# Optimization experiments

Hardware: AMD Instinct MI355X
Metric: run time of the kernel (lower is better)

Reference implementation:

```python
import jax, jax.numpy as jnp
import numpy as np

N_HEADS = 8
N_POINTS = 4
EPS = 1e-5


def _conv1x1(x, w, b):
    # x: [B,C,H,W], w: [O,C]
    return jnp.einsum('bchw,oc->bohw', x, w) + b[None, :, None, None]


def _gn(x, g, b, groups=32):
    B, C, H, W = x.shape
    xr = x.reshape(B, groups, C // groups, H, W)
    m = xr.mean((2, 3, 4), keepdims=True)
    v = xr.var((2, 3, 4), keepdims=True)
    xn = ((xr - m) * jax.lax.rsqrt(v + EPS)).reshape(B, C, H, W)
    return xn * g[None, :, None, None] + b[None, :, None, None]


def _ln(x, g, b):
    m = x.mean(-1, keepdims=True)
    v = x.var(-1, keepdims=True)
    return (x - m) * jax.lax.rsqrt(v + EPS) * g + b


def _ln_spec(x, g2, b2, n):
    # modality-specific LayerNorm: separate params for v tokens [:n] and i tokens [n:]
    return jnp.concatenate([_ln(x[:, :n], g2[0], b2[0]), _ln(x[:, n:], g2[1], b2[1])], 1)


def _sine_pos(h, w, d):
    nf = d // 2
    scale = 2.0 * np.pi
    ye = jnp.arange(1, h + 1, dtype=jnp.float32) / h * scale
    xe = jnp.arange(1, w + 1, dtype=jnp.float32) / w * scale
    dim_t = 10000.0 ** (2.0 * (jnp.arange(nf) // 2).astype(jnp.float32) / nf)
    def enc(e):
        p = e[:, None] / dim_t
        return jnp.stack([jnp.sin(p[:, 0::2]), jnp.cos(p[:, 1::2])], -1).reshape(e.shape[0], nf)
    py = enc(ye)  # [h,nf]
    px = enc(xe)  # [w,nf]
    pos = jnp.concatenate([jnp.broadcast_to(py[:, None, :], (h, w, nf)),
                           jnp.broadcast_to(px[None, :, :], (h, w, nf))], -1)
    return pos.reshape(h * w, d)


def _bilinear(vl, loc):
    # vl: [B,h,w,Hd,Dh] value for one level, loc: [B,Lq,Hd,P,2] normalized (x,y)
    B, h, w, Hd, Dh = vl.shape
    Lq, P = loc.shape[1], loc.shape[3]
    x = loc[..., 0] * w - 0.5
    y = loc[..., 1] * h - 0.5
    x0 = jnp.floor(x)
    y0 = jnp.floor(y)
    wx = x - x0
    wy = y - y0
    x0i = x0.astype(jnp.int32)
    y0i = y0.astype(jnp.int32)
    v2 = vl.reshape(B, h * w, Hd, Dh).transpose(0, 2, 1, 3)  # [B,Hd,HW,Dh]
    def g(ix, iy):
        valid = ((ix >= 0) & (ix < w) & (iy >= 0) & (iy < h)).astype(vl.dtype)
        flat = jnp.clip(iy, 0, h - 1) * w + jnp.clip(ix, 0, w - 1)  # [B,Lq,Hd,P]
        idx = flat.transpose(0, 2, 1, 3).reshape(B, Hd, Lq * P)
        gv = jnp.take_along_axis(v2, idx[..., None], axis=2)  # [B,Hd,Lq*P,Dh]
        gv = gv.reshape(B, Hd, Lq, P, Dh).transpose(0, 2, 1, 3, 4)  # [B,Lq,Hd,P,Dh]
        return gv * valid[..., None]
    return (g(x0i, y0i) * ((1 - wx) * (1 - wy))[..., None]
            + g(x0i + 1, y0i) * (wx * (1 - wy))[..., None]
            + g(x0i, y0i + 1) * ((1 - wx) * wy)[..., None]
            + g(x0i + 1, y0i + 1) * (wx * wy)[..., None])


def _deform_attn(q, src, ref, shapes, ow, ob, aww, awb, vw, vb, opw, opb):
    B, Len, D = src.shape
    L = len(shapes)
    Hd, P = N_HEADS, N_POINTS
    Dh = D // Hd
    value = src @ vw + vb
    off = (q @ ow + ob).reshape(B, Len, Hd, L, P, 2)
    aw = jax.nn.softmax((q @ aww + awb).reshape(B, Len, Hd, L * P), -1).reshape(B, Len, Hd, L, P)
    norm = jnp.array([[s[1], s[0]] for s in shapes], jnp.float32)  # (w,h) per level
    loc = ref[None, :, None, None, None, :] + off / norm[None, None, None, :, None, :]
    out = jnp.zeros((B, Len, Hd, Dh), value.dtype)
    start = 0
    for l, (hh, ww) in enumerate(shapes):
        vl = value[:, start:start + hh * ww].reshape(B, hh, ww, Hd, Dh)
        samp = _bilinear(vl, loc[:, :, :, l])  # [B,Len,Hd,P,Dh]
        out = out + (samp * aw[:, :, :, l, :, None]).sum(3)
        start += hh * ww
    return out.reshape(B, Len, D) @ opw + opb


def _forward(input_v, input_i, av_w, av_b, av_g, av_be, ai_w, ai_b, ai_g, ai_be,
             level_embed, off_w, off_b, aw_w, aw_b, vp_w, vp_b, op_w, op_b,
             ln1_g, ln1_b, ffn1_w, ffn1_b, ffn2_w, ffn2_b, ln2_g, ln2_b,
             as_w, as_b, as_g, as_be):
    b, c, h, w = input_v.shape
    D = av_w.shape[0]
    hw = h * w
    fv = _gn(_conv1x1(input_v, av_w, av_b), av_g, av_be)
    fi = _gn(_conv1x1(input_i, ai_w, ai_b), ai_g, ai_be)
    sv = fv.reshape(b, D, hw).transpose(0, 2, 1)
    si = fi.reshape(b, D, hw).transpose(0, 2, 1)
    src = jnp.concatenate([sv, si], 1)  # [b, 2hw, D]
    pos = _sine_pos(h, w, D)
    posf = jnp.concatenate([pos + level_embed[0], pos + level_embed[1]], 0)
    gx = (jnp.arange(w, dtype=jnp.float32) + 0.5) / w
    gy = (jnp.arange(h, dtype=jnp.float32) + 0.5) / h
    X, Y = jnp.meshgrid(gx, gy)
    ref1 = jnp.stack([X, Y], -1).reshape(hw, 2)
    ref = jnp.concatenate([ref1, ref1], 0)  # [2hw, 2]
    shapes = [(h, w), (h, w)]
    for i in range(off_w.shape[0]):
        q = src + posf
        attn = _deform_attn(q, src, ref, shapes, off_w[i], off_b[i], aw_w[i], aw_b[i],
                            vp_w[i], vp_b[i], op_w[i], op_b[i])
        src = _ln_spec(src + attn, ln1_g[i], ln1_b[i], hw)
        ff = jax.nn.relu(src @ ffn1_w[i] + ffn1_b[i]) @ ffn2_w[i] + ffn2_b[i]
        src = _ln_spec(src + ff, ln2_g[i], ln2_b[i], hw)
    out = src[:, :hw] + src[:, hw:]  # chunk along tokens, sum modalities
    out = out.transpose(0, 2, 1).reshape(b, D, h, w)
    return _gn(_conv1x1(out, as_w, as_b), as_g, as_be)


def setup_inputs():
    key = jax.random.key(0)
    B, C, H, W = 16, 768, 20, 20
    D, NL, Hd, L, P, Dff = 512, 6, N_HEADS, 2, N_POINTS, 1024
    ks = iter(jax.random.split(key, 64))
    def rn(shape, scale=0.02):
        return jax.random.normal(next(ks), shape, jnp.float32) * scale
    return {
        'input_v': jax.random.normal(next(ks), (B, C, H, W), jnp.float32),
        'input_i': jax.random.normal(next(ks), (B, C, H, W), jnp.float32),
        'av_w': rn((D, C)), 'av_b': jnp.zeros((D,)), 'av_g': jnp.ones((D,)), 'av_be': jnp.zeros((D,)),
        'ai_w': rn((D, C)), 'ai_b': jnp.zeros((D,)), 'ai_g': jnp.ones((D,)), 'ai_be': jnp.zeros((D,)),
        'level_embed': rn((L, D)),
        'off_w': rn((NL, D, Hd * L * P * 2)), 'off_b': rn((NL, Hd * L * P * 2), 0.5),
        'aw_w': rn((NL, D, Hd * L * P)), 'aw_b': jnp.zeros((NL, Hd * L * P)),
        'vp_w': rn((NL, D, D)), 'vp_b': jnp.zeros((NL, D)),
        'op_w': rn((NL, D, D)), 'op_b': jnp.zeros((NL, D)),
        'ln1_g': jnp.ones((NL, 2, D)), 'ln1_b': jnp.zeros((NL, 2, D)),
        'ffn1_w': rn((NL, D, Dff)), 'ffn1_b': jnp.zeros((NL, Dff)),
        'ffn2_w': rn((NL, Dff, D)), 'ffn2_b': jnp.zeros((NL, D)),
        'ln2_g': jnp.ones((NL, 2, D)), 'ln2_b': jnp.zeros((NL, 2, D)),
        'as_w': rn((C, D)), 'as_b': jnp.zeros((C,)), 'as_g': jnp.ones((C,)), 'as_be': jnp.zeros((C,)),
    }


def reference(input_v, input_i, av_w, av_b, av_g, av_be, ai_w, ai_b, ai_g, ai_be,
              level_embed, off_w, off_b, aw_w, aw_b, vp_w, vp_b, op_w, op_b,
              ln1_g, ln1_b, ffn1_w, ffn1_b, ffn2_w, ffn2_b, ln2_g, ln2_b,
              as_w, as_b, as_g, as_be):
    return _forward(input_v, input_i, av_w, av_b, av_g, av_be, ai_w, ai_b, ai_g, ai_be,
                    level_embed, off_w, off_b, aw_w, aw_b, vp_w, vp_b, op_w, op_b,
                    ln1_g, ln1_b, ffn1_w, ffn1_b, ffn2_w, ffn2_b, ln2_g, ln2_b,
                    as_w, as_b, as_g, as_be)
```

## Files before the change

kernel.cpp:

```cpp
#include <hip/hip_runtime.h>
#include <hip/hip_bf16.h>
#include <cstddef>
#include <math.h>


constexpr int kB   = 16;
constexpr int kCin = 768;
constexpr int kHW  = 400;
constexpr int kWpx = 20;
constexpr int kHpx = 20;
constexpr int kD   = 512;
constexpr int kLen = 800;
constexpr int kDff = 1024;
constexpr int kNL  = 6;
constexpr float kEps = 1e-5f;

typedef __attribute__((ext_vector_type(8))) short s8v;
typedef __attribute__((ext_vector_type(4))) short s4v;
typedef __attribute__((ext_vector_type(4))) float f4v;

__device__ __forceinline__ int swzk(int row, int k) {
  return (k & ~31) | ((((k >> 3) + (row >> 1)) & 3) << 3) | (k & 7);
}

__device__ __forceinline__ unsigned short f2b(float f) {
  union { __hip_bfloat16 h; unsigned short u; } cv;
  cv.h = __float2bfloat16(f);
  return cv.u;
}

__device__ __forceinline__ float b2f(unsigned short u) {
  return __uint_as_float(((unsigned)u) << 16);
}

__device__ __forceinline__ void gll(const unsigned short* g, unsigned short* l) {
  __builtin_amdgcn_global_load_lds(
      (const __attribute__((address_space(1))) unsigned int*)g,
      (__attribute__((address_space(3))) unsigned int*)l, 16, 0, 0);
}

__device__ __forceinline__ void breduce2(float& s, float& s2, float* sh) {
#pragma unroll
  for (int o = 32; o > 0; o >>= 1) {
    s  += __shfl_down(s, o);
    s2 += __shfl_down(s2, o);
  }
  const int wid = threadIdx.x >> 6, lane = threadIdx.x & 63;
  if (lane == 0) { sh[wid] = s; sh[4 + wid] = s2; }
  __syncthreads();
  if (threadIdx.x == 0) {
    sh[0] = sh[0] + sh[1] + sh[2] + sh[3];
    sh[4] = sh[4] + sh[5] + sh[6] + sh[7];
  }
  __syncthreads();
  s = sh[0]; s2 = sh[4];
}

template<int EPI>
__global__ __launch_bounds__(256)
void mgemm(const unsigned short* __restrict__ Abf,
           const unsigned short* __restrict__ Bw,
           const float* __restrict__ bias,
           const unsigned short* __restrict__ resb,
           float* __restrict__ Cf, unsigned short* __restrict__ Cb2,
           const float* __restrict__ aux,
           unsigned short* __restrict__ Cb,
           int K, int ldc, int Nreal)
{
  __shared__ unsigned short As[3][4096];
  __shared__ unsigned short Bs[3][4096];
  const int tid = threadIdx.x;
  const int w = tid >> 6, l = tid & 63;

  const int gx = gridDim.x;
  const int nwg = gx * gridDim.y;
  const int bid = blockIdx.y * gx + blockIdx.x;
  const int q = nwg >> 3, r = nwg & 7;
  const int xcd = bid & 7, idx = bid >> 3;
  const int wgid = (xcd < r ? xcd * (q + 1) : r * (q + 1) + (xcd - r) * q) + idx;
  const int m0 = (wgid / gx) * 128;
  const int n0 = (wgid % gx) * 128;

  if (EPI == 6 && m0 >= 6400) { Bw = resb; bias = aux; }

  f4v acc[4][4] = {};

  const int srow = w * 32 + (l >> 2);
  const unsigned short* ga0 = Abf + (size_t)(m0 + srow) * K + (l & 3) * 8;
  const unsigned short* ga1 = ga0 + (size_t)16 * K;
  const unsigned short* gb0 = Bw + (size_t)(n0 + srow) * K + (l & 3) * 8;
  const unsigned short* gb1 = gb0 + (size_t)16 * K;
  const int lb0 = (w * 32) * 32;
  const int lb1 = (w * 32 + 16) * 32;

  int aoff[4], boff[4];
#pragma unroll
  for (int f = 0; f < 4; f++) {
    const int ra = (w >> 1) * 64 + f * 16 + (l & 15);
    aoff[f] = ra * 32 + ((((l >> 4) + (ra >> 1)) & 3) << 3);
    const int rb = (w & 1) * 64 + f * 16 + (l & 15);
    boff[f] = rb * 32 + ((((l >> 4) + (rb >> 1)) & 3) << 3);
  }

#define STAGE(ko, bi) do { \
    gll(ga0 + (ko), &As[bi][lb0]); gll(ga1 + (ko), &As[bi][lb1]); \
    gll(gb0 + (ko), &Bs[bi][lb0]); gll(gb1 + (ko), &Bs[bi][lb1]); } while (0)

  const int NT = K >> 5;
  STAGE(0, 0);
  STAGE(32, 1);

  int cur = 0;
  int bpre = 2;
  int kpre = 64;
  for (int t = 0; t < NT; ++t) {
    if (t + 1 < NT) asm volatile("s_waitcnt vmcnt(4)" ::: "memory");
    else            asm volatile("s_waitcnt vmcnt(0)" ::: "memory");
    __builtin_amdgcn_s_barrier();
    __builtin_amdgcn_sched_barrier(0);
    if (t + 2 < NT) STAGE(kpre, bpre);
    s8v af[4], bf4[4];
#pragma unroll
    for (int f = 0; f < 4; f++) {
      af[f]  = *(const s8v*)&As[cur][aoff[f]];
      bf4[f] = *(const s8v*)&Bs[cur][boff[f]];
    }
    __builtin_amdgcn_s_setprio(1);
#pragma unroll
    for (int i = 0; i < 4; i++)
#pragma unroll
      for (int j = 0; j < 4; j++)
        acc[i][j] = __builtin_amdgcn_mfma_f32_16x16x32_bf16(af[i], bf4[j], acc[i][j], 0, 0, 0);
    __builtin_amdgcn_s_setprio(0);
    kpre += 32;
    bpre = (bpre == 2) ? 0 : bpre + 1;
    cur  = (cur == 2) ? 0 : cur + 1;
  }
#undef STAGE

  const int colb = n0 + (w & 1) * 64;
  const int rowb = m0 + (w >> 1) * 64 + (l >> 4) * 4;
#pragma unroll
  for (int i = 0; i < 4; i++) {
#pragma unroll
    for (int j = 0; j < 4; j++) {
      const int col = colb + j * 16 + (l & 15);
      float bv;
      if (EPI == 4) bv = (col < kD) ? bias[col] : 0.0f;
      else          bv = bias[col];
#pragma unroll
      for (int r2 = 0; r2 < 4; r2++) {
        const int row = rowb + i * 16 + r2;
        float v = acc[i][j][r2] + bv;
        if (EPI == 1) {
          Cb[(size_t)row * ldc + swzk(row, col)] = f2b(fmaxf(v, 0.0f));
        } else if (EPI == 2) {
          v += b2f(resb[(size_t)row * kD + swzk(row, col)]);
          Cb[(size_t)row * kD + col] = f2b(v);
        } else if (EPI == 3) {
          const int bb = row / kHW, p = row % kHW;
          Cf[((size_t)bb * Nreal + col) * kHW + p] = v;
        } else if (EPI == 4) {
          if (col < kD) {
            Cb[(size_t)row * kD + col] = f2b(v);
          } else {
            const int c = col - kD;
            if (c < 192)
              Cb2[(size_t)row * 192 + c] = f2b(v + aux[(size_t)(row % kLen) * 192 + c]);
          }
        } else if (EPI == 5) {
          if (row < kLen) {
            const int ll = col >> 8, c = col & 255;
            if (c < 192)
              Cf[(((size_t)ll * kLen) + row) * 192 + c] = v;
          }
        } else {
          Cb[(size_t)row * kD + col] = f2b(v);
        }
      }
    }
  }
}

__device__ __forceinline__ void cvt8t(const float* __restrict__ W,
                                      unsigned short* __restrict__ out,
                                      int K, int N, int g)
{
  const int n = g % N;
  const int k = (g / N) * 8;
  s8v p;
#pragma unroll
  for (int j = 0; j < 8; j++) p[j] = (short)f2b(W[(size_t)(k + j) * N + n]);
  const int base = n * K + (k & ~31) + ((((k >> 3) + (n >> 1)) & 3) << 3);
  *(s8v*)&out[base] = p;
}

__global__ __launch_bounds__(256)
void cvt_all_k(const float* __restrict__ vp_w, const float* __restrict__ op_w,
               const float* __restrict__ off_w, const float* __restrict__ aw_w,
               const float* __restrict__ f1w_a, const float* __restrict__ f2w_a,
               unsigned short* __restrict__ wall)
{
  const int lyr = blockIdx.x / 832;
  int g = (blockIdx.x % 832) * 256 + threadIdx.x;
  unsigned short* wl = wall + (size_t)lyr * 1703936;
  if (g < 32768) { cvt8t(vp_w + (size_t)lyr * kD * kD, wl, 512, 512, g); return; }
  g -= 32768;
  if (g < 16384) {
    const int n = g & 255;
    const int k = (g >> 8) * 8;
    const float* ow  = off_w + (size_t)lyr * kD * 128;
    const float* aww = aw_w  + (size_t)lyr * kD * 64;
    s8v p;
#pragma unroll
    for (int j = 0; j < 8; j++) {
      float v = 0.0f;
      if (n < 128)      v = ow[(size_t)(k + j) * 128 + n];
      else if (n < 192) v = aww[(size_t)(k + j) * 64 + (n - 128)];
      p[j] = (short)f2b(v);
    }
    const int row = 512 + n;
    const int base = row * 512 + (k & ~31) + ((((k >> 3) + (row >> 1)) & 3) << 3);
    *(s8v*)&wl[base] = p;
    return;
  }
  g -= 16384;
  if (g < 32768) { cvt8t(op_w + (size_t)lyr * kD * kD, wl + 393216, 512, 512, g); return; }
  g -= 32768;
  if (g < 65536) { cvt8t(f1w_a + (size_t)lyr * kD * kDff, wl + 655360, 512, 1024, g); return; }
  g -= 65536;
  cvt8t(f2w_a + (size_t)lyr * kDff * kD, wl + 1179648, 1024, 512, g);
}

__global__ __launch_bounds__(256)
void pre_k(const float* __restrict__ level_embed,
           const float* __restrict__ off_w, const float* __restrict__ aw_w,
           const float* __restrict__ off_b, const float* __restrict__ aw_b,
           unsigned short* __restrict__ posfb,
           unsigned short* __restrict__ woaw_all, float* __restrict__ biasall)
{
  int g = blockIdx.x * 256 + threadIdx.x;
  if (g < 57344) {
    const int d0 = (g & 63) * 8;
    const int t  = g >> 6;
    s8v o;
    if (t >= kLen) {
#pragma unroll
      for (int j = 0; j < 8; j++) o[j] = 0;
    } else {
      const int lvl = t / kHW;
      const int tt = t % kHW;
      const int yy = tt / kWpx, xx = tt % kWpx;
#pragma unroll
      for (int j = 0; j < 8; j++) {
        const int d = d0 + j;
        const int dd = d & 255;
        const float e = (d < 256) ? ((float)(yy + 1) * (6.283185307179586f / kHpx))
                                  : ((float)(xx + 1) * (6.283185307179586f / kWpx));
        const float dimt = powf(10000.0f, (float)(dd >> 1) / 128.0f);
        const float pp = e / dimt;
        const float val = (dd & 1) ? cosf(pp) : sinf(pp);
        o[j] = (short)f2b(val + level_embed[lvl * kD + d]);
      }
    }
    *(s8v*)&posfb[(size_t)t * kD + swzk(t, d0)] = o;
    return;
  }
  g -= 57344;
  if (g < 98304) {
    const int l = g >> 14;
    const int gg = g & 16383;
    const int n = gg & 255;
    const int k = (gg >> 8) * 8;
    const float* ow = off_w + (size_t)l * kD * 128;
    const float* aww = aw_w + (size_t)l * kD * 64;
    s8v p;
#pragma unroll
    for (int j = 0; j < 8; j++) {
      float v = 0.0f;
      if (n < 128)      v = ow[(size_t)(k + j) * 128 + n];
      else if (n < 192) v = aww[(size_t)(k + j) * 64 + (n - 128)];
      p[j] = (short)f2b(v);
    }
    const int row = l * 256 + n;
    const int base = row * 512 + (k & ~31) + ((((k >> 3) + (row >> 1)) & 3) << 3);
    *(s8v*)&woaw_all[base] = p;
    return;
  }
  g -= 98304;
  if (g < 1536) {
    const int l = g >> 8, c = g & 255;
    float v = 0.0f;
    if (c < 128)      v = off_b[l * 128 + c];
    else if (c < 192) v = aw_b[l * 64 + (c - 128)];
    biasall[l * 256 + c] = v;
  }
}

__global__ void cvtw_d_k(const float* __restrict__ W, unsigned short* __restrict__ out,
                         int K, int N)
{
  const int gid = blockIdx.x * 256 + threadIdx.x;
  const int K8 = K >> 3;
  const int n  = gid / K8;
  const int k  = (gid % K8) * 8;
  s8v p;
#pragma unroll
  for (int j = 0; j < 8; j++) p[j] = (short)f2b(W[(size_t)n * K + k + j]);
  const int base = n * K + (k & ~31) + ((((k >> 3) + (n >> 1)) & 3) << 3);
  *(s8v*)&out[base] = p;
}

__global__ void tincvt_k(const float* __restrict__ inv, const float* __restrict__ ini,
                         const float* __restrict__ W0, const float* __restrict__ W1,
                         unsigned short* __restrict__ out, unsigned short* __restrict__ wcs)
{
  __shared__ float t[16][17];
  const int bid = blockIdx.x;
  if (bid < 38400) {
    const int z = bid / 1200;
    const int rem = bid % 1200;
    const int c0 = (rem % 48) * 16, p0 = (rem / 48) * 16;
    const int mod = z >> 4, b = z & 15;
    const float* in = (mod ? ini : inv) + (size_t)b * kCin * kHW;
    const int tx = threadIdx.x & 15, ty = threadIdx.x >> 4;
    t[ty][tx] = in[((size_t)(c0 + ty)) * kHW + p0 + tx];
    __syncthreads();
    const int row = z * kHW + p0 + ty;
    const int c = c0 + tx;
    out[(size_t)row * kCin + swzk(row, c)] = f2b(t[tx][ty]);
    return;
  }
  int gid = (bid - 38400) * 256 + threadIdx.x;
  const float* W = W0;
  unsigned short* o = wcs;
  if (gid >= 49152) { gid -= 49152; W = W1; o = wcs + 393216; }
  const int n = gid / 96;
  const int k = (gid % 96) * 8;
  s8v p;
#pragma unroll
  for (int j = 0; j < 8; j++) p[j] = (short)f2b(W[(size_t)n * kCin + k + j]);
  const int base = n * kCin + (k & ~31) + ((((k >> 3) + (n >> 1)) & 3) << 3);
  *(s8v*)&o[base] = p;
}

__global__ __launch_bounds__(256)
void gn_stats_tok_k(const unsigned short* __restrict__ x, float* __restrict__ stats)
{
  __shared__ float sh[8];
  const int mb = blockIdx.x >> 5;
  const int g = blockIdx.x & 31;
  const unsigned short* xb = x + (size_t)mb * kHW * kD + g * 16;
  float s = 0.f, s2 = 0.f;
  for (int i = threadIdx.x; i < 800; i += 256) {
    const int p = i >> 1, half = i & 1;
    const s8v u = *(const s8v*)&xb[(size_t)p * kD + half * 8];
#pragma unroll
    for (int j = 0; j < 8; j++) {
      const float v = b2f((unsigned short)u[j]);
      s += v; s2 += v * v;
    }
  }
  breduce2(s, s2, sh);
  if (threadIdx.x == 0) {
    const float mean = s / (kHW * 16.0f);
    const float var  = s2 / (kHW * 16.0f) - mean * mean;
    stats[blockIdx.x * 2]     = mean;
    stats[blockIdx.x * 2 + 1] = rsqrtf(var + kEps);
  }
}

__global__ void gn_norm_tok_k(const unsigned short* __restrict__ x,
                              unsigned short* __restrict__ srcb,
                              const float* __restrict__ stats,
                              const float* __restrict__ gv, const float* __restrict__ bev,
                              const float* __restrict__ gi, const float* __restrict__ bei)
{
  const int gid = blockIdx.x * 256 + threadIdx.x;
  const int d0 = (gid & 63) * 8;
  const int rl = gid >> 6;
  const int mb = rl / kHW;
  const int p  = rl - mb * kHW;
  const int mod = mb >> 4, b = mb & 15;
  const int g = d0 >> 4;
  const float mean = stats[(mb * 32 + g) * 2];
  const float rstd = stats[(mb * 32 + g) * 2 + 1];
  const float* gam = mod ? gi : gv;
  const float* bet = mod ? bei : bev;
  const s8v u = *(const s8v*)&x[(size_t)rl * kD + d0];
  const int row = b * kLen + mod * kHW + p;
  s8v o;
#pragma unroll
  for (int j = 0; j < 8; j++)
    o[j] = (short)f2b((b2f((unsigned short)u[j]) - mean) * rstd * gam[d0 + j] + bet[d0 + j]);
  *(s8v*)&srcb[(size_t)row * kD + swzk(row, d0)] = o;
}

__global__ __launch_bounds__(256)
void gn_stats_ch_k(const float* __restrict__ x, float* __restrict__ stats)
{
  __shared__ float sh[8];
  const int b = blockIdx.x >> 5;
  const int g = blockIdx.x & 31;
  const float* xb = x + (size_t)b * kCin * kHW + (size_t)g * 24 * kHW;
  float s = 0.f, s2 = 0.f;
  for (int i = threadIdx.x; i < 24 * kHW; i += 256) {
    const float v = xb[i];
    s += v; s2 += v * v;
  }
  breduce2(s, s2, sh);
  if (threadIdx.x == 0) {
    const float mean = s / (24.0f * kHW);
    const float var  = s2 / (24.0f * kHW) - mean * mean;
    stats[blockIdx.x * 2]     = mean;
    stats[blockIdx.x * 2 + 1] = rsqrtf(var + kEps);
  }
}

__global__ void gn_norm_ch_k(const float* __restrict__ x, float* __restrict__ out,
                             const float* __restrict__ stats,
                             const float* __restrict__ gam, const float* __restrict__ bet)
{
  const int idx = blockIdx.x * 256 + threadIdx.x;
  const int rest = idx / kHW;
  const int c = rest % kCin;
  const int b = rest / kCin;
  const int g = c / 24;
  const float mean = stats[(b * 32 + g) * 2];
  const float rstd = stats[(b * 32 + g) * 2 + 1];
  out[idx] = (x[idx] - mean) * rstd * gam[c] + bet[c];
}

__global__ __launch_bounds__(256)
void ln4_k(const unsigned short* __restrict__ x, unsigned short* __restrict__ outb,
           const float* __restrict__ gamma, const float* __restrict__ beta)
{
  const int row = blockIdx.x * 4 + (threadIdx.x >> 6);
  const int l = threadIdx.x & 63;
  const int mod = ((row % kLen) < kHW) ? 0 : 1;
  const s8v u = *(const s8v*)&x[(size_t)row * kD + l * 8];
  float v[8];
#pragma unroll
  for (int j = 0; j < 8; j++) v[j] = b2f((unsigned short)u[j]);
  float s = 0.f, s2 = 0.f;
#pragma unroll
  for (int j = 0; j < 8; j++) { s += v[j]; s2 += v[j] * v[j]; }
#pragma unroll
  for (int o = 32; o > 0; o >>= 1) {
    s  += __shfl_xor(s, o);
    s2 += __shfl_xor(s2, o);
  }
  const float mean = s * (1.0f / kD);
  const float var  = s2 * (1.0f / kD) - mean * mean;
  const float rstd = rsqrtf(var + kEps);
  const float* g  = gamma + mod * kD + l * 8;
  const float* be = beta  + mod * kD + l * 8;
  s8v o8;
#pragma unroll
  for (int j = 0; j < 8; j++)
    o8[j] = (short)f2b((v[j] - mean) * rstd * g[j] + be[j]);
  *(s8v*)&outb[(size_t)row * kD + swzk(row, l * 8)] = o8;
}

__global__ __launch_bounds__(256)
void sample_k(const unsigned short* __restrict__ value,
              const unsigned short* __restrict__ offaw,
              unsigned short* __restrict__ out)
{
  __shared__ float wls[2][64][8];
  const int tid = threadIdx.x;
  const int tok = tid >> 7;
  const int wt  = tid & 127;
  const int token = blockIdx.x * 2 + tok;
  const int b = token / kLen;
  const int t = token % kLen;
  const int tt = t % kHW;

  if (wt < 64) {
    const int h = wt >> 3, lp = wt & 7, lvl = lp >> 2, p = lp & 3;
    const unsigned short* oa = offaw + (size_t)token * 192;
    const float lg = b2f(oa[128 + h * 8 + lp]);
    float mx = lg;
#pragma unroll
    for (int msk = 1; msk < 8; msk <<= 1) mx = fmaxf(mx, __shfl_xor(mx, msk));
    const float ex = __expf(lg - mx);
    float ssum = ex;
#pragma unroll
    for (int msk = 1; msk < 8; msk <<= 1) ssum += __shfl_xor(ssum, msk);
    const float aw = ex / ssum;

    const float x = (float)(tt % kWpx) + b2f(oa[h * 16 + lvl * 8 + p * 2]);
    const float y = (float)(tt / kWpx) + b2f(oa[h * 16 + lvl * 8 + p * 2 + 1]);
    const float x0f = floorf(x), y0f = floorf(y);
    const float wx = x - x0f, wy = y - y0f;
    const int x0 = (int)x0f, y0 = (int)y0f;
    const int rowbase = b * kLen + lvl * kHW;
#pragma unroll
    for (int dy = 0; dy < 2; dy++) {
#pragma unroll
      for (int dx = 0; dx < 2; dx++) {
        const int ix = x0 + dx, iy = y0 + dy;
        const bool valid = (ix >= 0) & (ix < kWpx) & (iy >= 0) & (iy < kHpx);
        const float cw = (dx ? wx : 1.0f - wx) * (dy ? wy : 1.0f - wy);
        const float w = valid ? aw * cw : 0.0f;
        const int ixc = min(max(ix, 0), kWpx - 1);
        const int iyc = min(max(iy, 0), kHpx - 1);
        const int r = rowbase + iyc * kWpx + ixc;
        const int cn = dy * 2 + dx;
        wls[tok][wt][cn * 2]     = w;
        wls[tok][wt][cn * 2 + 1] = __int_as_float(r);
      }
    }
  }
  __syncthreads();

  const int c0 = wt * 4;
  const int h = wt >> 4;
  float acc0 = 0.f, acc1 = 0.f, acc2 = 0.f, acc3 = 0.f;
  const unsigned short* vb = value + c0;
#pragma unroll
  for (int pp = 0; pp < 8; pp++) {
    const float* wl = wls[tok][h * 8 + pp];
#pragma unroll
    for (int cn = 0; cn < 4; cn++) {
      const float w = wl[cn * 2];
      const int r = __float_as_int(wl[cn * 2 + 1]);
      const s4v q = *(const s4v*)(vb + (size_t)r * kD);
      acc0 += w * b2f((unsigned short)q[0]);
      acc1 += w * b2f((unsigned short)q[1]);
      acc2 += w * b2f((unsigned short)q[2]);
      acc3 += w * b2f((unsigned short)q[3]);
    }
  }
  const int sk = swzk(token, c0);
  s4v o;
  o[0] = (short)f2b(acc0); o[1] = (short)f2b(acc1);
  o[2] = (short)f2b(acc2); o[3] = (short)f2b(acc3);
  *(s4v*)&out[(size_t)token * kD + sk] = o;
}

__global__ void sumtok_k(const unsigned short* __restrict__ srcb,
                         unsigned short* __restrict__ tokb)
{
  const int gid = blockIdx.x * 256 + threadIdx.x;
  const int d0 = (gid & 63) * 8;
  const int rest = gid >> 6;
  const int b = rest / kHW, p = rest % kHW;
  const int r1 = b * kLen + p;
  const int r2 = r1 + kHW;
  const int ro = b * kHW + p;
  const s8v u1 = *(const s8v*)&srcb[(size_t)r1 * kD + swzk(r1, d0)];
  const s8v u2 = *(const s8v*)&srcb[(size_t)r2 * kD + swzk(r2, d0)];
  s8v o;
#pragma unroll
  for (int j = 0; j < 8; j++)
    o[j] = (short)f2b(b2f((unsigned short)u1[j]) + b2f((unsigned short)u2[j]));
  *(s8v*)&tokb[(size_t)ro * kD + swzk(ro, d0)] = o;
}

extern "C" void kernel_launch(void* const* d_in, const int* in_sizes, int n_in,
                              void* d_out, int out_size, void* d_ws, size_t ws_size,
                              hipStream_t stream)
{
  const float* input_v     = (const float*)d_in[0];
  const float* input_i     = (const float*)d_in[1];
  const float* av_w        = (const float*)d_in[2];
  const float* av_b        = (const float*)d_in[3];
  const float* av_g        = (const float*)d_in[4];
  const float* av_be       = (const float*)d_in[5];
  const float* ai_w        = (const float*)d_in[6];
  const float* ai_b        = (const float*)d_in[7];
  const float* ai_g        = (const float*)d_in[8];
  const float* ai_be       = (const float*)d_in[9];
  const float* level_embed = (const float*)d_in[10];
  const float* off_w       = (const float*)d_in[11];
  const float* off_b       = (const float*)d_in[12];
  const float* aw_w        = (const float*)d_in[13];
  const float* aw_b        = (const float*)d_in[14];
  const float* vp_w        = (const float*)d_in[15];
  const float* vp_b        = (const float*)d_in[16];
  const float* op_w        = (const float*)d_in[17];
  const float* op_b        = (const float*)d_in[18];
  const float* ln1_g       = (const float*)d_in[19];
  const float* ln1_b       = (const float*)d_in[20];
  const float* ffn1_w      = (const float*)d_in[21];
  const float* ffn1_b      = (const float*)d_in[22];
  const float* ffn2_w      = (const float*)d_in[23];
  const float* ffn2_b      = (const float*)d_in[24];
  const float* ln2_g       = (const float*)d_in[25];
  const float* ln2_b       = (const float*)d_in[26];
  const float* as_w        = (const float*)d_in[27];
  const float* as_b        = (const float*)d_in[28];
  const float* as_g        = (const float*)d_in[29];
  const float* as_be       = (const float*)d_in[30];

  unsigned short* offawb = (unsigned short*)d_ws;
  float* posWc   = (float*)(offawb + 2457600);
  float* biasall = posWc   + (size_t)921600;
  float* stats   = biasall + (size_t)1536;
  unsigned short* srcb     = (unsigned short*)(stats + 2048);
  unsigned short* bufA     = srcb     + (size_t)6553600;
  unsigned short* bufB     = bufA     + (size_t)13107200;
  unsigned short* wall     = bufB     + (size_t)6553600;
  unsigned short* wcs      = wall     + (size_t)10223616;
  unsigned short* woaw_all = wcs      + (size_t)786432;
  unsigned short* posfb    = woaw_all + (size_t)786432;
  float* wallf = (float*)wall;

  const int M = kB * kLen;

  pre_k<<<dim3(614), 256, 0, stream>>>(level_embed, off_w, aw_w, off_b, aw_b,
                                       posfb, woaw_all, biasall);
  mgemm<5><<<dim3(12, 7), 256, 0, stream>>>(
      posfb, woaw_all, biasall, nullptr, posWc, nullptr, nullptr, nullptr,
      512, 0, 0);

  tincvt_k<<<dim3(38784), 256, 0, stream>>>(input_v, input_i, av_w, ai_w,
                                            bufA, wcs);
  mgemm<6><<<dim3(4, 100), 256, 0, stream>>>(
      bufA, wcs, av_b, wcs + 393216, nullptr, nullptr, ai_b, bufB, 768, 512, 0);
  gn_stats_tok_k<<<dim3(1024), 256, 0, stream>>>(bufB, stats);
  gn_norm_tok_k<<<dim3(3200), 256, 0, stream>>>(
      bufB, srcb, stats, av_g, av_be, ai_g, ai_be);

  cvt_all_k<<<dim3(4992), 256, 0, stream>>>(vp_w, op_w, off_w, aw_w,
                                            ffn1_w, ffn2_w, wall);

  for (int l = 0; l < kNL; l++) {
    unsigned short* wcomb = wall + (size_t)l * 1703936;
    unsigned short* wop   = wcomb + 393216;
    unsigned short* wf1   = wcomb + 655360;
    unsigned short* wf2   = wcomb + 1179648;
    const float* vbl  = vp_b   + (size_t)l * kD;
    const float* opbl = op_b   + (size_t)l * kD;
    const float* l1g  = ln1_g  + (size_t)l * 2 * kD;
    const float* l1b  = ln1_b  + (size_t)l * 2 * kD;
    const float* f1b  = ffn1_b + (size_t)l * kDff;
    const float* f2b_ = ffn2_b + (size_t)l * kD;
    const float* l2g  = ln2_g  + (size_t)l * 2 * kD;
    const float* l2b  = ln2_b  + (size_t)l * 2 * kD;

    mgemm<4><<<dim3(6, 100), 256, 0, stream>>>(
        srcb, wcomb, vbl, nullptr, nullptr, offawb, posWc + (size_t)l * 153600,
        bufA, 512, 0, 0);

    sample_k<<<dim3(M / 2), 256, 0, stream>>>(bufA, offawb, bufB);

    mgemm<2><<<dim3(4, 100), 256, 0, stream>>>(
        bufB, wop, opbl, srcb, nullptr, nullptr, nullptr, bufA, 512, 512, 0);

    ln4_k<<<dim3(M / 4), 256, 0, stream>>>(bufA, srcb, l1g, l1b);

    mgemm<1><<<dim3(8, 100), 256, 0, stream>>>(
        srcb, wf1, f1b, nullptr, nullptr, nullptr, nullptr, bufA, 512, 1024, 0);
    mgemm<2><<<dim3(4, 100), 256, 0, stream>>>(
        bufA, wf2, f2b_, srcb, nullptr, nullptr, nullptr, bufB, 1024, 512, 0);

    ln4_k<<<dim3(M / 4), 256, 0, stream>>>(bufB, srcb, l2g, l2b);
  }

  sumtok_k<<<dim3(1600), 256, 0, stream>>>(srcb, bufA);
  cvtw_d_k<<<dim3(192), 256, 0, stream>>>(as_w, wcs, 512, 768);
  mgemm<3><<<dim3(6, 50), 256, 0, stream>>>(
      bufA, wcs, as_b, nullptr, wallf, nullptr, nullptr, nullptr, 512, 0, 768);
  gn_stats_ch_k<<<dim3(kB * 32), 256, 0, stream>>>(wallf, stats);
  gn_norm_ch_k<<<dim3(19200), 256, 0, stream>>>(
      wallf, (float*)d_out, stats, as_g, as_be);
}
```

Baseline: 1.085 ms.

## Fuse residual add and modality LayerNorm into full-row GEMM epilogue

Adds a GEMM kernel where each block computes 32 rows across the full 512-column width, so the residual add, bias, and modality-specific LayerNorm can run in the epilogue using cross-wave partial sums in shared memory. It replaces the out-projection and FFN2 GEMMs plus their separate LayerNorm kernels, removing two launches and a bf16 intermediate round trip per layer. In exchange, each block reloads the whole B weight panel for only 32 rows, giving lower arithmetic intensity and fewer blocks (400). It also uses double buffering with an extra barrier per k-step. The output is written in place over the residual buffer.

New measurement: 1.332 ms. 1.23x slower.

```diff
diff --git a/kernel.cpp b/kernel.cpp
--- a/kernel.cpp
+++ b/kernel.cpp
@@ -102,13 +102,13 @@
     boff[f] = rb * 32 + ((((l >> 4) + (rb >> 1)) & 3) << 3);
   }
 
-#define STAGE(ko, bi) do { \
+#define STAGEG(ko, bi) do { \
     gll(ga0 + (ko), &As[bi][lb0]); gll(ga1 + (ko), &As[bi][lb1]); \
     gll(gb0 + (ko), &Bs[bi][lb0]); gll(gb1 + (ko), &Bs[bi][lb1]); } while (0)
 
   const int NT = K >> 5;
-  STAGE(0, 0);
-  STAGE(32, 1);
+  STAGEG(0, 0);
+  STAGEG(32, 1);
 
   int cur = 0;
   int bpre = 2;
@@ -118,7 +118,7 @@
     else            asm volatile("s_waitcnt vmcnt(0)" ::: "memory");
     __builtin_amdgcn_s_barrier();
     __builtin_amdgcn_sched_barrier(0);
-    if (t + 2 < NT) STAGE(kpre, bpre);
+    if (t + 2 < NT) STAGEG(kpre, bpre);
     s8v af[4], bf4[4];
 #pragma unroll
     for (int f = 0; f < 4; f++) {
@@ -136,7 +136,7 @@
     bpre = (bpre == 2) ? 0 : bpre + 1;
     cur  = (cur == 2) ? 0 : cur + 1;
   }
-#undef STAGE
+#undef STAGEG
 
   const int colb = n0 + (w & 1) * 64;
   const int rowb = m0 + (w >> 1) * 64 + (l >> 4) * 4;
@@ -154,9 +154,6 @@
         float v = acc[i][j][r2] + bv;
         if (EPI == 1) {
           Cb[(size_t)row * ldc + swzk(row, col)] = f2b(fmaxf(v, 0.0f));
-        } else if (EPI == 2) {
-          v += b2f(resb[(size_t)row * kD + swzk(row, col)]);
-          Cb[(size_t)row * kD + col] = f2b(v);
         } else if (EPI == 3) {
           const int bb = row / kHW, p = row % kHW;
           Cf[((size_t)bb * Nreal + col) * kHW + p] = v;
@@ -182,6 +179,151 @@
   }
 }
 
+__global__ __launch_bounds__(256)
+void mgemm_ln(const unsigned short* __restrict__ Abf,
+              const unsigned short* __restrict__ Bw,
+              const float* __restrict__ bias,
+              const unsigned short* __restrict__ resb,
+              const float* __restrict__ gamma, const float* __restrict__ beta,
+              unsigned short* __restrict__ outb, int K)
+{
+  __shared__ unsigned short LDS[2][17920];
+  __shared__ float part[32][8];
+  const int tid = threadIdx.x;
+  const int w = tid >> 6, l = tid & 63;
+  const int m0 = blockIdx.x * 32;
+
+  f4v acc[2][8] = {};
+
+  int aoff[2], boff[8];
+#pragma unroll
+  for (int i = 0; i < 2; i++) {
+    const int ra = i * 16 + (l & 15);
+    aoff[i] = 16384 + ra * 32 + ((((l >> 4) + (ra >> 1)) & 3) << 3);
+  }
+#pragma unroll
+  for (int j = 0; j < 8; j++) {
+    const int rb = w * 128 + j * 16 + (l & 15);
+    boff[j] = rb * 32 + ((((l >> 4) + (rb >> 1)) & 3) << 3);
+  }
+
+  const unsigned short* gsrcB = Bw + (size_t)(l >> 2) * K + (l & 3) * 8;
+  const unsigned short* gsrcA = Abf + (size_t)(m0 + (l >> 2)) * K + (l & 3) * 8;
+
+  auto STAGE = [&](int k0, int bi) {
+    if (w == 0) {
+      gll(gsrcA + k0, &LDS[bi][16384]);
+      gll(gsrcA + (size_t)16 * K + k0, &LDS[bi][16384 + 512]);
+#pragma unroll
+      for (int c = 0; c < 7; c++)
+        gll(gsrcB + (size_t)(c * 16) * K + k0, &LDS[bi][c * 512]);
+    } else if (w == 1) {
+#pragma unroll
+      for (int c = 7; c < 16; c++)
+        gll(gsrcB + (size_t)(c * 16) * K + k0, &LDS[bi][c * 512]);
+    } else if (w == 2) {
+#pragma unroll
+      for (int c = 16; c < 25; c++)
+        gll(gsrcB + (size_t)(c * 16) * K + k0, &LDS[bi][c * 512]);
+    } else {
+#pragma unroll
+      for (int c = 25; c < 32; c++)
+        gll(gsrcB + (size_t)(c * 16) * K + k0, &LDS[bi][c * 512]);
+    }
+  };
+
+  const int NT = K >> 5;
+  STAGE(0, 0);
+  STAGE(32, 1);
+  for (int t = 0; t < NT; ++t) {
+    if (t + 1 < NT) {
+      if (w == 3) asm volatile("s_waitcnt vmcnt(7)" ::: "memory");
+      else        asm volatile("s_waitcnt vmcnt(9)" ::: "memory");
+    } else {
+      asm volatile("s_waitcnt vmcnt(0)" ::: "memory");
+    }
+    __builtin_amdgcn_s_barrier();
+    __builtin_amdgcn_sched_barrier(0);
+    const int cur = t & 1;
+    s8v af[2], bf8[8];
+#pragma unroll
+    for (int i = 0; i < 2; i++) af[i] = *(const s8v*)&LDS[cur][aoff[i]];
+#pragma unroll
+    for (int j = 0; j < 8; j++) bf8[j] = *(const s8v*)&LDS[cur][boff[j]];
+    __builtin_amdgcn_s_setprio(1);
+#pragma unroll
+    for (int i = 0; i < 2; i++)
+#pragma unroll
+      for (int j = 0; j < 8; j++)
+        acc[i][j] = __builtin_amdgcn_mfma_f32_16x16x32_bf16(af[i], bf8[j], acc[i][j], 0, 0, 0);
+    __builtin_amdgcn_s_setprio(0);
+    asm volatile("s_waitcnt lgkmcnt(0)" ::: "memory");
+    __builtin_amdgcn_s_barrier();
+    __builtin_amdgcn_sched_barrier(0);
+    if (t + 2 < NT) STAGE((t + 2) * 32, cur);
+  }
+
+  const int lg = l & 15, gq = l >> 4;
+  float bcol[8], g0c[8], g1c[8], b0c[8], b1c[8];
+#pragma unroll
+  for (int j = 0; j < 8; j++) {
+    const int col = w * 128 + j * 16 + lg;
+    bcol[j] = bias[col];
+    g0c[j] = gamma[col];  g1c[j] = gamma[kD + col];
+    b0c[j] = beta[col];   b1c[j] = beta[kD + col];
+  }
+#pragma unroll
+  for (int i = 0; i < 2; i++)
+#pragma unroll
+    for (int r = 0; r < 4; r++) {
+      const int row = m0 + i * 16 + gq * 4 + r;
+#pragma unroll
+      for (int j = 0; j < 8; j++) {
+        const int col = w * 128 + j * 16 + lg;
+        acc[i][j][r] += bcol[j] + b2f(resb[(size_t)row * kD + swzk(row, col)]);
+      }
+    }
+#pragma unroll
+  for (int i = 0; i < 2; i++)
+#pragma unroll
+    for (int r = 0; r < 4; r++) {
+      float p = 0.f, p2 = 0.f;
+#pragma unroll
+      for (int j = 0; j < 8; j++) { const float v = acc[i][j][r]; p += v; p2 += v * v; }
+#pragma unroll
+      for (int msk = 1; msk < 16; msk <<= 1) {
+        p  += __shfl_xor(p, msk);
+        p2 += __shfl_xor(p2, msk);
+      }
+      if (lg == 0) {
+        part[i * 16 + gq * 4 + r][w]     = p;
+        part[i * 16 + gq * 4 + r][4 + w] = p2;
+      }
+    }
+  __syncthreads();
+#pragma unroll
+  for (int i = 0; i < 2; i++)
+#pragma unroll
+    for (int r = 0; r < 4; r++) {
+      const int rl = i * 16 + gq * 4 + r;
+      const float s  = part[rl][0] + part[rl][1] + part[rl][2] + part[rl][3];
+      const float s2 = part[rl][4] + part[rl][5] + part[rl][6] + part[rl][7];
+      const float mean = s * (1.0f / kD);
+      const float var  = s2 * (1.0f / kD) - mean * mean;
+      const float rstd = rsqrtf(var + kEps);
+      const int row = m0 + rl;
+      const int mod = ((row % kLen) < kHW) ? 0 : 1;
+#pragma unroll
+      for (int j = 0; j < 8; j++) {
+        const int col = w * 128 + j * 16 + lg;
+        const float gg = mod ? g1c[j] : g0c[j];
+        const float bb = mod ? b1c[j] : b0c[j];
+        outb[(size_t)row * kD + swzk(row, col)] =
+            f2b((acc[i][j][r] - mean) * rstd * gg + bb);
+      }
+    }
+}
+
 __device__ __forceinline__ void cvt8t(const float* __restrict__ W,
                                       unsigned short* __restrict__ out,
                                       int K, int N, int g)
@@ -429,37 +571,6 @@
   const float mean = stats[(b * 32 + g) * 2];
   const float rstd = stats[(b * 32 + g) * 2 + 1];
   out[idx] = (x[idx] - mean) * rstd * gam[c] + bet[c];
-}
-
-__global__ __launch_bounds__(256)
-void ln4_k(const unsigned short* __restrict__ x, unsigned short* __restrict__ outb,
-           const float* __restrict__ gamma, const float* __restrict__ beta)
-{
-  const int row = blockIdx.x * 4 + (threadIdx.x >> 6);
-  const int l = threadIdx.x & 63;
-  const int mod = ((row % kLen) < kHW) ? 0 : 1;
-  const s8v u = *(const s8v*)&x[(size_t)row * kD + l * 8];
-  float v[8];
-#pragma unroll
-  for (int j = 0; j < 8; j++) v[j] = b2f((unsigned short)u[j]);
-  float s = 0.f, s2 = 0.f;
-#pragma unroll
-  for (int j = 0; j < 8; j++) { s += v[j]; s2 += v[j] * v[j]; }
-#pragma unroll
-  for (int o = 32; o > 0; o >>= 1) {
-    s  += __shfl_xor(s, o);
-    s2 += __shfl_xor(s2, o);
-  }
-  const float mean = s * (1.0f / kD);
-  const float var  = s2 * (1.0f / kD) - mean * mean;
-  const float rstd = rsqrtf(var + kEps);
-  const float* g  = gamma + mod * kD + l * 8;
-  const float* be = beta  + mod * kD + l * 8;
-  s8v o8;
-#pragma unroll
-  for (int j = 0; j < 8; j++)
-    o8[j] = (short)f2b((v[j] - mean) * rstd * g[j] + be[j]);
-  *(s8v*)&outb[(size_t)row * kD + swzk(row, l * 8)] = o8;
 }
 
 __global__ __launch_bounds__(256)
@@ -646,17 +757,14 @@
 
     sample_k<<<dim3(M / 2), 256, 0, stream>>>(bufA, offawb, bufB);
 
-    mgemm<2><<<dim3(4, 100), 256, 0, stream>>>(
-        bufB, wop, opbl, srcb, nullptr, nullptr, nullptr, bufA, 512, 512, 0);
-
-    ln4_k<<<dim3(M / 4), 256, 0, stream>>>(bufA, srcb, l1g, l1b);
+    mgemm_ln<<<dim3(M / 32), 256, 0, stream>>>(
+        bufB, wop, opbl, srcb, l1g, l1b, srcb, 512);
 
     mgemm<1><<<dim3(8, 100), 256, 0, stream>>>(
         srcb, wf1, f1b, nullptr, nullptr, nullptr, nullptr, bufA, 512, 1024, 0);
-    mgemm<2><<<dim3(4, 100), 256, 0, stream>>>(
-        bufA, wf2, f2b_, srcb, nullptr, nullptr, nullptr, bufB, 1024, 512, 0);
-
-    ln4_k<<<dim3(M / 4), 256, 0, stream>>>(bufB, srcb, l2g, l2b);
+
+    mgemm_ln<<<dim3(M / 32), 256, 0, stream>>>(
+        bufA, wf2, f2b_, srcb, l2g, l2b, srcb, 1024);
   }
 
   sumtok_k<<<dim3(1600), 256, 0, stream>>>(srcb, bufA);
```
